# Kernel tuning notes

Hardware: AMD Instinct MI355X
Metric: run time of the kernel (lower is better)

Reference implementation:

```python
import jax, jax.numpy as jnp
import numpy as np

ALPHA = 10.0
DELTA = 0.0005
N = 16777216  # array_length


def setup_inputs() -> dict:
    key = jax.random.key(0)
    k1, k2 = jax.random.split(key)
    # learned parameter: in the original module this is initialized to linspace(0,1,N);
    # we use uniform [0,1] so the piecewise-linear search path is non-degenerate.
    indices = jax.random.uniform(k1, (N,), dtype=jnp.float32)
    array = jax.random.normal(k2, (N,), dtype=jnp.float32)
    return {"indices": indices, "array": array}


def reference(indices, array):
    # clamp learned knot positions to [0, 1]
    clamped = jnp.clip(indices, 0.0, 1.0)
    # piecewise-linear function f with x-knots = clamped, y-values = array.
    # jnp.interp requires ascending knots, so sort (x, y) pairs by x.
    order = jnp.argsort(clamped)
    xs = clamped[order]
    ys = array[order]
    # vectorized version of the per-index loop:
    #   left_item = f(clamped[i-1] + delta), this_item = f(clamped[i] - delta)
    q_left = clamped[:-1] + DELTA   # [N-1]
    q_this = clamped[1:] - DELTA    # [N-1]
    f_left = jnp.interp(q_left, xs, ys)
    f_this = jnp.interp(q_this, xs, ys)
    gap = jnp.maximum(f_left - f_this, 0.0)
    return ALPHA * jnp.sum(gap)
```

## Files before the change

kernel.cpp:

```cpp
#include <hip/hip_runtime.h>
#include <stdint.h>

#define ALPHA_C 10.0f
#define DELTA_C 0.0005f

typedef unsigned long long u64;
typedef unsigned u32;
typedef unsigned short u16;

#define KB2   (1u << 22)
#define NREG  8192
#define FPR   512
#define NBK   4096
#define RPB   2
#define FPB   1024
#define CAPB  4800
#define ACHUNK 32768
#define Q38MAX ((1ULL << 38) - 1)

#define OLDKB (1u << 22)
#define SCAN_BLOCKS 1024
#define SCAN_TPB 256
#define SCAN_PER_THREAD 16

__device__ __forceinline__ float clamp01(float x) {
    return fminf(fmaxf(x, 0.0f), 1.0f);
}
__device__ __forceinline__ u64 q38_of(float x) {
    double d = (double)clamp01(x) * 274877906944.0;
    u64 q = (u64)d;
    return q > Q38MAX ? Q38MAX : q;
}
__device__ __forceinline__ u16 f2bf(float f) {
    u32 b = __float_as_uint(f);
    return (u16)((b + 0x8000u) >> 16);
}
__device__ __forceinline__ float bf2f(u32 h) {
    return __uint_as_float(h << 16);
}


__global__ void __launch_bounds__(256) k_hist(const float* __restrict__ ind,
                                              u32* __restrict__ cnt8k, int n) {
    __shared__ u32 lh[NREG];
    for (int k = threadIdx.x; k < (int)NREG; k += 256) lh[k] = 0;
    __syncthreads();
    int stride = gridDim.x * blockDim.x;
    for (int i = blockIdx.x * blockDim.x + threadIdx.x; i < n; i += stride)
        atomicAdd(&lh[(u32)(q38_of(ind[i]) >> 25)], 1u);
    __syncthreads();
    for (int k = threadIdx.x; k < (int)NREG; k += 256) {
        u32 v = lh[k];
        if (v) atomicAdd(&cnt8k[k], v);
    }
}

__global__ void __launch_bounds__(1024) k_scan8k(u32* __restrict__ cnt8k) {
    __shared__ u32 lds[1024];
    int tid = threadIdx.x;
    int base = tid * 8;
    u32 v[8]; u32 tot = 0;
#pragma unroll
    for (int k = 0; k < 8; ++k) { v[k] = cnt8k[base + k]; tot += v[k]; }
    lds[tid] = tot;
    __syncthreads();
    u32 x = tot;
    for (int s = 1; s < 1024; s <<= 1) {
        u32 y = (tid >= s) ? lds[tid - s] : 0u;
        __syncthreads();
        x += y; lds[tid] = x;
        __syncthreads();
    }
    u32 run = x - tot;
#pragma unroll
    for (int k = 0; k < 8; ++k) { u32 c = v[k]; cnt8k[base + k] = run; run += c; }
}

__global__ void k_prep(const u32* __restrict__ cnt8k, u32* __restrict__ bcur) {
    int b = blockIdx.x * 256 + threadIdx.x;
    if (b < (int)NBK) bcur[b] = cnt8k[b * RPB];
}

__global__ void __launch_bounds__(256) k_bucket(const float* __restrict__ ind,
                                                u32* __restrict__ bcur,
                                                u64* __restrict__ rec, int n) {
    __shared__ u32 hist[NBK];
    __shared__ u32 base[NBK];
    int cbase = blockIdx.x * ACHUNK;
    for (u32 k = threadIdx.x; k < (u32)NBK; k += 256) hist[k] = 0;
    __syncthreads();
    for (int k = threadIdx.x; k < ACHUNK; k += 256) {
        int i = cbase + k;
        if (i >= n) break;
        u32 bk = (u32)(q38_of(ind[i]) >> 26);
        atomicAdd(&hist[bk], 1u);
    }
    __syncthreads();
    for (u32 k = threadIdx.x; k < (u32)NBK; k += 256) {
        u32 h = hist[k];
        base[k] = h ? atomicAdd(&bcur[k], h) : 0u;
    }
    __syncthreads();
    for (int k = threadIdx.x; k < ACHUNK; k += 256) {
        int i = cbase + k;
        if (i >= n) break;
        u64 q = q38_of(ind[i]);
        u32 bk = (u32)(q >> 26);
        u32 d = atomicAdd(&base[bk], 1u);
        rec[d] = (q << 24) | (u64)(u32)i;
    }
}

__global__ void __launch_bounds__(256) k_group_fine(const u32* __restrict__ cnt8k,
                                                    const float* __restrict__ arr,
                                                    u16* __restrict__ foff16,
                                                    u64* __restrict__ rec, int n) {
    __shared__ u64 srec[CAPB];
    __shared__ u32 sc[FPB];
    __shared__ u32 lad[256];
    int b = blockIdx.x;
    u32 S = cnt8k[b * RPB];
    u32 E = (b * RPB + RPB < (int)NREG) ? cnt8k[b * RPB + RPB] : (u32)n;
    u32 cnt = E - S; if (cnt > CAPB) cnt = CAPB;
    for (u32 j = threadIdx.x; j < cnt; j += 256) srec[j] = rec[S + j];
    for (u32 f = threadIdx.x; f < (u32)FPB; f += 256) sc[f] = 0;
    __syncthreads();
    for (u32 j = threadIdx.x; j < cnt; j += 256) {
        u32 fb = (u32)(srec[j] >> 40) & (FPB - 1);
        atomicAdd(&sc[fb], 1u);
    }
    __syncthreads();
    u32 c0 = sc[threadIdx.x * 4 + 0], c1 = sc[threadIdx.x * 4 + 1];
    u32 c2 = sc[threadIdx.x * 4 + 2], c3 = sc[threadIdx.x * 4 + 3];
    u32 tsum = c0 + c1 + c2 + c3;
    lad[threadIdx.x] = tsum;
    __syncthreads();
    u32 x = tsum;
    for (int st = 1; st < 256; st <<= 1) {
        u32 y = (threadIdx.x >= (u32)st) ? lad[threadIdx.x - st] : 0u;
        __syncthreads();
        x += y; lad[threadIdx.x] = x;
        __syncthreads();
    }
    u32 ex = x - tsum;
    u32 e0 = ex, e1 = ex + c0, e2 = ex + c0 + c1, e3 = ex + c0 + c1 + c2;
    sc[threadIdx.x * 4 + 0] = e0; sc[threadIdx.x * 4 + 1] = e1;
    sc[threadIdx.x * 4 + 2] = e2; sc[threadIdx.x * 4 + 3] = e3;
    __syncthreads();
    {
        u32 fb0 = threadIdx.x * 4;
        u32 rs0 = sc[fb0 & ~511u];
        u32 gb  = (u32)b * FPB + fb0;
        foff16[gb + 0] = (u16)(e0 + c0 - rs0);
        foff16[gb + 1] = (u16)(e1 + c1 - rs0);
        foff16[gb + 2] = (u16)(e2 + c2 - rs0);
        foff16[gb + 3] = (u16)(e3 + c3 - rs0);
    }
    __syncthreads();
    for (u32 j = threadIdx.x; j < cnt; j += 256) {
        u64 v = srec[j];
        u32 fb  = (u32)(v >> 40) & (FPB - 1);
        u32 i   = (u32)(v & 0xFFFFFFu);
        u32 xlo = (u32)(v >> 24) & 0xFFFFu;
        u32 ybf = f2bf(arr[i]);
        u32 pos = atomicAdd(&sc[fb], 1u);
        rec[S + pos] = ((u64)xlo << 40) | ((u64)ybf << 24) | (u64)i;
    }
}

__device__ __forceinline__ void bucket_range(u32 b, const u32* __restrict__ cnt8k,
                                             const u16* __restrict__ foff16,
                                             u32* s, u32* e) {
    u32 r = b >> 9;
    u32 rbase = cnt8k[r];
    u32 lb = b & (FPR - 1);
    *s = rbase + (lb ? (u32)foff16[b - 1] : 0u);
    *e = rbase + (u32)foff16[b];
}

__device__ float feval_q(u64 qq, const u32* __restrict__ cnt8k,
                         const u16* __restrict__ foff16, const u64* __restrict__ fdata) {
    u32 qb = (u32)(qq >> 16);
    u32 ql = (u32)(qq & 0xFFFFu);
    u32 s, e;
    bucket_range(qb, cnt8k, foff16, &s, &e);
    long long loK = -1;
    u64 hiK = ~0ULL;
    float loY = 0.0f, hiY = 0.0f;
    for (u32 p = s; p < e; ++p) {
        u64 d = fdata[p];
        u32 xlo = (u32)(d >> 40);
        u64 key = ((((u64)qb << 16) | xlo) << 24) | (d & 0xFFFFFFULL);
        float y = bf2f((u32)(d >> 24) & 0xFFFFu);
        if (xlo <= ql) { if ((long long)key >= loK) { loK = (long long)key; loY = y; } }
        else           { if (key < hiK)             { hiK = key;            hiY = y; } }
    }
    if (loK < 0) {
        u32 bl = qb;
        while (bl > 0) {
            --bl;
            u32 s2, e2;
            bucket_range(bl, cnt8k, foff16, &s2, &e2);
            if (e2 > s2) {
                for (u32 p = s2; p < e2; ++p) {
                    u64 d = fdata[p];
                    u64 key = ((((u64)bl << 16) | (d >> 40)) << 24) | (d & 0xFFFFFFULL);
                    if ((long long)key >= loK) { loK = (long long)key; loY = bf2f((u32)(d >> 24) & 0xFFFFu); }
                }
                break;
            }
        }
    }
    if (hiK == ~0ULL) {
        u32 br = qb;
        while (br < KB2 - 1) {
            ++br;
            u32 s2, e2;
            bucket_range(br, cnt8k, foff16, &s2, &e2);
            if (e2 > s2) {
                for (u32 p = s2; p < e2; ++p) {
                    u64 d = fdata[p];
                    u64 key = ((((u64)br << 16) | (d >> 40)) << 24) | (d & 0xFFFFFFULL);
                    if (key < hiK) { hiK = key; hiY = bf2f((u32)(d >> 24) & 0xFFFFu); }
                }
                break;
            }
        }
    }
    if (loK < 0) return hiY;
    if (hiK == ~0ULL) return loY;
    u64 loQ = (u64)loK >> 24;
    u64 hiQ = hiK >> 24;
    if (hiQ == loQ) return loY;
    float dq = (float)(qq - loQ);
    float dd = (float)(hiQ - loQ);
    return loY + (dq / dd) * (hiY - loY);
}

__global__ void __launch_bounds__(512) k_eval(const u32* __restrict__ cnt8k,
        const u16* __restrict__ foff16, const u64* __restrict__ fdata,
        u32* __restrict__ oval, int n) {
    __shared__ u32 fend[FPR];
    int r = blockIdx.x;
    u32 s = cnt8k[r];
    u32 e = (r + 1 < (int)NREG) ? cnt8k[r + 1] : (u32)n;
    fend[threadIdx.x] = s + (u32)foff16[r * FPR + threadIdx.x];
    __syncthreads();
    for (u32 t = s + threadIdx.x; t < e; t += 512) {
        u64 d = fdata[t];
        u32 lo = 0;
#pragma unroll
        for (u32 st = 256; st; st >>= 1) if (t >= fend[lo + st - 1]) lo += st;
        u64 xq = (((u64)((u32)r * FPR + lo)) << 16) | (d >> 40);
        u32 i = (u32)(d & 0xFFFFFFu);
        float x = (float)((double)xq * 3.63797880709171295e-12);
        float qpf = x + DELTA_C;
        float qmf = x - DELTA_C;
        u64 qp = q38_of(qpf);
        u64 qm = q38_of(qmf);
        float fp = feval_q(qp, cnt8k, foff16, fdata);
        float fm = feval_q(qm, cnt8k, foff16, fdata);
        oval[i] = ((u32)f2bf(fp) << 16) | (u32)f2bf(fm);
    }
}

__global__ void __launch_bounds__(256) k_pair2(const u32* __restrict__ oval,
                                               float* __restrict__ out, int n) {
    int stride = gridDim.x * blockDim.x;
    float sum = 0.0f;
    for (int j = blockIdx.x * blockDim.x + threadIdx.x; j < n - 1; j += stride) {
        u32 a = oval[j], b = oval[j + 1];
        sum += fmaxf(bf2f(a >> 16) - bf2f(b & 0xFFFFu), 0.0f);
    }
    float w = sum;
    for (int s = 32; s > 0; s >>= 1) w += __shfl_down(w, s, 64);
    __shared__ float wsum[4];
    if ((threadIdx.x & 63) == 0) wsum[threadIdx.x >> 6] = w;
    __syncthreads();
    if (threadIdx.x == 0)
        atomicAdd(out, ALPHA_C * (wsum[0] + wsum[1] + wsum[2] + wsum[3]));
}


__device__ __forceinline__ int bucket_of(float x) {
    int b = (int)(x * (float)OLDKB);
    b = b < 0 ? 0 : b;
    b = b > (int)OLDKB - 1 ? (int)OLDKB - 1 : b;
    return b;
}

__global__ void scan1(u32* __restrict__ off, u32* __restrict__ bsums) {
    __shared__ u32 lds[SCAN_TPB];
    int base = blockIdx.x * (SCAN_TPB * SCAN_PER_THREAD) + threadIdx.x * SCAN_PER_THREAD;
    u32 v[SCAN_PER_THREAD];
    u32 tot = 0;
#pragma unroll
    for (int k = 0; k < SCAN_PER_THREAD; ++k) { v[k] = off[base + k]; tot += v[k]; }
    lds[threadIdx.x] = tot;
    __syncthreads();
    u32 x = tot;
    for (int s = 1; s < SCAN_TPB; s <<= 1) {
        u32 y = (threadIdx.x >= (u32)s) ? lds[threadIdx.x - s] : 0u;
        __syncthreads();
        x += y; lds[threadIdx.x] = x;
        __syncthreads();
    }
    if (threadIdx.x == SCAN_TPB - 1) bsums[blockIdx.x] = x;
    u32 run = x - tot;
#pragma unroll
    for (int k = 0; k < SCAN_PER_THREAD; ++k) { u32 c = v[k]; off[base + k] = run; run += c; }
}

__global__ void scan2(u32* __restrict__ bsums) {
    __shared__ u32 lds[SCAN_BLOCKS];
    int tid = threadIdx.x;
    u32 v = bsums[tid];
    lds[tid] = v;
    __syncthreads();
    u32 x = v;
    for (int s = 1; s < SCAN_BLOCKS; s <<= 1) {
        u32 y = (tid >= s) ? lds[tid - s] : 0u;
        __syncthreads();
        x += y; lds[tid] = x;
        __syncthreads();
    }
    bsums[tid] = x - v;
}

__global__ void scan3(u32* __restrict__ off, const u32* __restrict__ bsums) {
    int base = blockIdx.x * (SCAN_TPB * SCAN_PER_THREAD);
    u32 add = bsums[blockIdx.x];
#pragma unroll
    for (int k = 0; k < SCAN_PER_THREAD; ++k)
        off[base + k * SCAN_TPB + threadIdx.x] += add;
}

__global__ void hist_kernel(const float* __restrict__ ind, u32* __restrict__ off, int n) {
    int i = blockIdx.x * blockDim.x + threadIdx.x;
    if (i < n) atomicAdd(&off[bucket_of(clamp01(ind[i]))], 1u);
}

__global__ void scatter_kernel(const float* __restrict__ ind, const float* __restrict__ arr,
                               u32* __restrict__ off, float2* __restrict__ buck, int n) {
    int i = blockIdx.x * blockDim.x + threadIdx.x;
    if (i < n) {
        float x = clamp01(ind[i]);
        u32 p = atomicAdd(&off[bucket_of(x)], 1u);
        buck[p] = make_float2(x, arr[i]);
    }
}

__device__ float feval(float q, const u32* __restrict__ off, const float2* __restrict__ buck) {
    int b = bucket_of(q);
    u32 s = (b == 0) ? 0u : off[b - 1];
    u32 e = off[b];
    float loX = -1e30f, loY = 0.0f, hiX = 1e30f, hiY = 0.0f;
    for (u32 u = s; u < e; ++u) {
        float2 p = buck[u];
        if (p.x <= q) { if (p.x >= loX) { loX = p.x; loY = p.y; } }
        else          { if (p.x <  hiX) { hiX = p.x; hiY = p.y; } }
    }
    if (loX == -1e30f) {
        int bl = b;
        while (bl > 0) {
            --bl;
            u32 s2 = (bl == 0) ? 0u : off[bl - 1];
            u32 e2 = off[bl];
            if (e2 > s2) {
                for (u32 u = s2; u < e2; ++u) {
                    float2 p = buck[u];
                    if (p.x >= loX) { loX = p.x; loY = p.y; }
                }
                break;
            }
        }
    }
    if (hiX == 1e30f) {
        int br = b;
        while (br < (int)OLDKB - 1) {
            ++br;
            u32 s2 = off[br - 1];
            u32 e2 = off[br];
            if (e2 > s2) {
                for (u32 u = s2; u < e2; ++u) {
                    float2 p = buck[u];
                    if (p.x < hiX) { hiX = p.x; hiY = p.y; }
                }
                break;
            }
        }
    }
    if (loX == -1e30f) return hiY;
    if (hiX ==  1e30f) return loY;
    return loY + (q - loX) * (hiY - loY) / (hiX - loX);
}

__global__ void query_kernel(const float* __restrict__ ind, const u32* __restrict__ off,
                             const float2* __restrict__ buck, float* __restrict__ out, int nterm) {
    int j = blockIdx.x * blockDim.x + threadIdx.x;
    float term = 0.0f;
    if (j < nterm) {
        float c0 = clamp01(ind[j]);
        float c1 = clamp01(ind[j + 1]);
        float fa = feval(c0 + DELTA_C, off, buck);
        float fb = feval(c1 - DELTA_C, off, buck);
        term = fmaxf(fa - fb, 0.0f);
    }
    float w = term;
    for (int s = 32; s > 0; s >>= 1) w += __shfl_down(w, s, 64);
    __shared__ float wsum[4];
    if ((threadIdx.x & 63) == 0) wsum[threadIdx.x >> 6] = w;
    __syncthreads();
    if (threadIdx.x == 0) atomicAdd(out, ALPHA_C * (wsum[0] + wsum[1] + wsum[2] + wsum[3]));
}


extern "C" void kernel_launch(void* const* d_in, const int* in_sizes, int n_in,
                              void* d_out, int out_size, void* d_ws, size_t ws_size,
                              hipStream_t stream) {
    const float* ind = (const float*)d_in[0];
    const float* arr = (const float*)d_in[1];
    float* out = (float*)d_out;
    int n = in_sizes[0];

    const int tpb = 256;
    int nblk = (n + tpb - 1) / tpb;
    uint8_t* w = (uint8_t*)d_ws;

    const size_t FOFF_SZ = (size_t)KB2 * 2;
    const size_t AUX = (size_t)1 << 20;
    size_t SZ8 = (size_t)n * 8, SZ4 = (size_t)n * 4;
    size_t base = FOFF_SZ + AUX;
    size_t need = base + SZ8 + SZ4;

    if (n <= (1 << 24) && ws_size >= need) {
        u16* foff16 = (u16*)w;
        u32* cnt8k  = (u32*)(w + FOFF_SZ);
        u32* bcur   = (u32*)(w + FOFF_SZ + 32768);
        u64* rec    = (u64*)(w + base);
        u32* oval   = (u32*)(w + base + SZ8);

        hipMemsetAsync(cnt8k, 0, NREG * 4, stream);
        hipMemsetAsync(out, 0, sizeof(float) * (size_t)out_size, stream);

        int abks = (n + ACHUNK - 1) / ACHUNK;
        k_hist<<<512, 256, 0, stream>>>(ind, cnt8k, n);
        k_scan8k<<<1, 1024, 0, stream>>>(cnt8k);
        k_prep<<<(NBK + 255) / 256, 256, 0, stream>>>(cnt8k, bcur);
        k_bucket<<<abks, 256, 0, stream>>>(ind, bcur, rec, n);
        k_group_fine<<<NBK, 256, 0, stream>>>(cnt8k, arr, foff16, rec, n);
        k_eval<<<NREG, 512, 0, stream>>>(cnt8k, foff16, rec, oval, n);
        k_pair2<<<2048, 256, 0, stream>>>(oval, out, n);
    } else {
        const size_t FO = (size_t)OLDKB * 4;
        u32* off = (u32*)w;
        u32* bsums = (u32*)(w + FO);
        float2* buck = (float2*)(w + FO + 4096);

        hipMemsetAsync(off, 0, FO, stream);
        hipMemsetAsync(out, 0, sizeof(float) * (size_t)out_size, stream);

        hist_kernel<<<nblk, tpb, 0, stream>>>(ind, off, n);
        scan1<<<SCAN_BLOCKS, SCAN_TPB, 0, stream>>>(off, bsums);
        scan2<<<1, SCAN_BLOCKS, 0, stream>>>(bsums);
        scan3<<<SCAN_BLOCKS, SCAN_TPB, 0, stream>>>(off, bsums);
        scatter_kernel<<<nblk, tpb, 0, stream>>>(ind, arr, off, buck, n);
        int nterm = n - 1;
        query_kernel<<<(nterm + tpb - 1) / tpb, tpb, 0, stream>>>(ind, off, buck, out, nterm);
    }
}
```

Measured before the change: 1.774 ms.

## Fully sort fine buckets and evaluate interp by rank with windowed offsets

Each fine bucket is now fully sorted in shared memory with an insertion sort, so lookups can find the rank of a query by counting keys at or below it in its bucket. The neighbouring knots are then the adjacent entries in the sorted array, which removes the min/max scans and the outward searches across empty buckets. k_eval loads bucket offsets for a window of nearby regions into shared memory. The y value is now gathered during bucketing rather than in the grouping pass. This relies on queries staying within the loaded window and on buckets being small enough for insertion sort to be cheap. It also reuses the oval buffer's memory for recy.

Result: slower. 1.869 ms (+5.4%).

```diff
diff --git a/kernel.cpp b/kernel.cpp
--- a/kernel.cpp
+++ b/kernel.cpp
@@ -16,6 +16,8 @@
 #define FPB   1024
 #define CAPB  4800
 #define ACHUNK 32768
+#define WR    5
+#define WMAXB ((2 * WR + 1) * FPR)
 #define Q38MAX ((1ULL << 38) - 1)
 
 #define OLDKB (1u << 22)
@@ -82,8 +84,10 @@
 }
 
 __global__ void __launch_bounds__(256) k_bucket(const float* __restrict__ ind,
+                                                const float* __restrict__ arr,
                                                 u32* __restrict__ bcur,
-                                                u64* __restrict__ rec, int n) {
+                                                u64* __restrict__ rec,
+                                                u16* __restrict__ recy, int n) {
     __shared__ u32 hist[NBK];
     __shared__ u32 base[NBK];
     int cbase = blockIdx.x * ACHUNK;
@@ -108,25 +112,26 @@
         u32 bk = (u32)(q >> 26);
         u32 d = atomicAdd(&base[bk], 1u);
         rec[d] = (q << 24) | (u64)(u32)i;
+        recy[d] = f2bf(arr[i]);
     }
 }
 
 __global__ void __launch_bounds__(256) k_group_fine(const u32* __restrict__ cnt8k,
-                                                    const float* __restrict__ arr,
+                                                    const u16* __restrict__ recy,
                                                     u16* __restrict__ foff16,
                                                     u64* __restrict__ rec, int n) {
-    __shared__ u64 srec[CAPB];
+    __shared__ u64 s2[CAPB];
+    __shared__ u16 sy[CAPB];
     __shared__ u32 sc[FPB];
     __shared__ u32 lad[256];
     int b = blockIdx.x;
     u32 S = cnt8k[b * RPB];
     u32 E = (b * RPB + RPB < (int)NREG) ? cnt8k[b * RPB + RPB] : (u32)n;
     u32 cnt = E - S; if (cnt > CAPB) cnt = CAPB;
-    for (u32 j = threadIdx.x; j < cnt; j += 256) srec[j] = rec[S + j];
     for (u32 f = threadIdx.x; f < (u32)FPB; f += 256) sc[f] = 0;
     __syncthreads();
     for (u32 j = threadIdx.x; j < cnt; j += 256) {
-        u32 fb = (u32)(srec[j] >> 40) & (FPB - 1);
+        u32 fb = (u32)(rec[S + j] >> 40) & (FPB - 1);
         atomicAdd(&sc[fb], 1u);
     }
     __syncthreads();
@@ -158,79 +163,52 @@
     }
     __syncthreads();
     for (u32 j = threadIdx.x; j < cnt; j += 256) {
-        u64 v = srec[j];
-        u32 fb  = (u32)(v >> 40) & (FPB - 1);
+        u64 v = rec[S + j];
+        u32 fb = (u32)(v >> 40) & (FPB - 1);
+        u32 p = atomicAdd(&sc[fb], 1u);
+        s2[p] = v;
+        sy[p] = recy[S + j];
+    }
+    __syncthreads();
+    for (u32 f = threadIdx.x; f < (u32)FPB; f += 256) {
+        u32 st = f ? sc[f - 1] : 0u;
+        u32 en = sc[f];
+        for (u32 a = st + 1; a < en; ++a) {
+            u64 key = s2[a]; u16 ky = sy[a]; u32 m = a;
+            while (m > st && s2[m - 1] > key) { s2[m] = s2[m - 1]; sy[m] = sy[m - 1]; --m; }
+            s2[m] = key; sy[m] = ky;
+        }
+    }
+    __syncthreads();
+    for (u32 j = threadIdx.x; j < cnt; j += 256) {
+        u64 v = s2[j];
         u32 i   = (u32)(v & 0xFFFFFFu);
         u32 xlo = (u32)(v >> 24) & 0xFFFFu;
-        u32 ybf = f2bf(arr[i]);
-        u32 pos = atomicAdd(&sc[fb], 1u);
-        rec[S + pos] = ((u64)xlo << 40) | ((u64)ybf << 24) | (u64)i;
-    }
-}
-
-__device__ __forceinline__ void bucket_range(u32 b, const u32* __restrict__ cnt8k,
-                                             const u16* __restrict__ foff16,
-                                             u32* s, u32* e) {
-    u32 r = b >> 9;
-    u32 rbase = cnt8k[r];
-    u32 lb = b & (FPR - 1);
-    *s = rbase + (lb ? (u32)foff16[b - 1] : 0u);
-    *e = rbase + (u32)foff16[b];
-}
-
-__device__ float feval_q(u64 qq, const u32* __restrict__ cnt8k,
-                         const u16* __restrict__ foff16, const u64* __restrict__ fdata) {
-    u32 qb = (u32)(qq >> 16);
+        u32 ybf = (u32)sy[j];
+        rec[S + j] = ((u64)xlo << 40) | ((u64)ybf << 24) | (u64)i;
+    }
+}
+
+__device__ __forceinline__ float feval2(u64 qq, u32 baseB, u32 nw,
+                                        const u32* pos,
+                                        const u64* __restrict__ fdata, u32 n) {
+    u32 wb = (u32)(qq >> 16) - baseB;
     u32 ql = (u32)(qq & 0xFFFFu);
-    u32 s, e;
-    bucket_range(qb, cnt8k, foff16, &s, &e);
-    long long loK = -1;
-    u64 hiK = ~0ULL;
-    float loY = 0.0f, hiY = 0.0f;
-    for (u32 p = s; p < e; ++p) {
-        u64 d = fdata[p];
-        u32 xlo = (u32)(d >> 40);
-        u64 key = ((((u64)qb << 16) | xlo) << 24) | (d & 0xFFFFFFULL);
-        float y = bf2f((u32)(d >> 24) & 0xFFFFu);
-        if (xlo <= ql) { if ((long long)key >= loK) { loK = (long long)key; loY = y; } }
-        else           { if (key < hiK)             { hiK = key;            hiY = y; } }
-    }
-    if (loK < 0) {
-        u32 bl = qb;
-        while (bl > 0) {
-            --bl;
-            u32 s2, e2;
-            bucket_range(bl, cnt8k, foff16, &s2, &e2);
-            if (e2 > s2) {
-                for (u32 p = s2; p < e2; ++p) {
-                    u64 d = fdata[p];
-                    u64 key = ((((u64)bl << 16) | (d >> 40)) << 24) | (d & 0xFFFFFFULL);
-                    if ((long long)key >= loK) { loK = (long long)key; loY = bf2f((u32)(d >> 24) & 0xFFFFu); }
-                }
-                break;
-            }
-        }
-    }
-    if (hiK == ~0ULL) {
-        u32 br = qb;
-        while (br < KB2 - 1) {
-            ++br;
-            u32 s2, e2;
-            bucket_range(br, cnt8k, foff16, &s2, &e2);
-            if (e2 > s2) {
-                for (u32 p = s2; p < e2; ++p) {
-                    u64 d = fdata[p];
-                    u64 key = ((((u64)br << 16) | (d >> 40)) << 24) | (d & 0xFFFFFFULL);
-                    if (key < hiK) { hiK = key; hiY = bf2f((u32)(d >> 24) & 0xFFFFu); }
-                }
-                break;
-            }
-        }
-    }
-    if (loK < 0) return hiY;
-    if (hiK == ~0ULL) return loY;
-    u64 loQ = (u64)loK >> 24;
-    u64 hiQ = hiK >> 24;
+    u32 bs = pos[wb], be = pos[wb + 1];
+    u32 c = 0;
+    for (u32 p = bs; p < be; ++p)
+        c += ((u32)(fdata[p] >> 40) <= ql) ? 1u : 0u;
+    u32 P = bs + c;
+    if (P == 0)  return bf2f((u32)(fdata[0] >> 24) & 0xFFFFu);
+    if (P >= n)  return bf2f((u32)(fdata[n - 1] >> 24) & 0xFFFFu);
+    u64 dlo = fdata[P - 1];
+    u64 dhi = fdata[P];
+    u32 wl = wb; while (wl > 0 && pos[wl] > P - 1) --wl;
+    u32 wh = wb; while (wh + 1 < nw && pos[wh + 1] <= P) ++wh;
+    u64 loQ = (((u64)(baseB + wl)) << 16) | (dlo >> 40);
+    u64 hiQ = (((u64)(baseB + wh)) << 16) | (dhi >> 40);
+    float loY = bf2f((u32)(dlo >> 24) & 0xFFFFu);
+    float hiY = bf2f((u32)(dhi >> 24) & 0xFFFFu);
     if (hiQ == loQ) return loY;
     float dq = (float)(qq - loQ);
     float dd = (float)(hiQ - loQ);
@@ -240,17 +218,27 @@
 __global__ void __launch_bounds__(512) k_eval(const u32* __restrict__ cnt8k,
         const u16* __restrict__ foff16, const u64* __restrict__ fdata,
         u32* __restrict__ oval, int n) {
-    __shared__ u32 fend[FPR];
+    __shared__ u32 pos[WMAXB + 1];
     int r = blockIdx.x;
+    int r0 = r - WR; if (r0 < 0) r0 = 0;
+    int r1 = r + WR; if (r1 > (int)NREG - 1) r1 = (int)NREG - 1;
+    u32 nw = (u32)(r1 - r0 + 1) << 9;
+    u32 baseB = (u32)r0 << 9;
+    for (u32 k = threadIdx.x; k < nw; k += 512) {
+        u32 reg = (u32)r0 + (k >> 9);
+        pos[1 + k] = cnt8k[reg] + (u32)foff16[(reg << 9) + (k & 511u)];
+    }
+    if (threadIdx.x == 0) pos[0] = cnt8k[r0];
+    __syncthreads();
     u32 s = cnt8k[r];
     u32 e = (r + 1 < (int)NREG) ? cnt8k[r + 1] : (u32)n;
-    fend[threadIdx.x] = s + (u32)foff16[r * FPR + threadIdx.x];
-    __syncthreads();
+    u32 selfoff = ((u32)(r - r0)) << 9;
     for (u32 t = s + threadIdx.x; t < e; t += 512) {
         u64 d = fdata[t];
         u32 lo = 0;
 #pragma unroll
-        for (u32 st = 256; st; st >>= 1) if (t >= fend[lo + st - 1]) lo += st;
+        for (u32 st = 256; st; st >>= 1)
+            if (t >= pos[selfoff + lo + st]) lo += st;
         u64 xq = (((u64)((u32)r * FPR + lo)) << 16) | (d >> 40);
         u32 i = (u32)(d & 0xFFFFFFu);
         float x = (float)((double)xq * 3.63797880709171295e-12);
@@ -258,9 +246,10 @@
         float qmf = x - DELTA_C;
         u64 qp = q38_of(qpf);
         u64 qm = q38_of(qmf);
-        float fp = feval_q(qp, cnt8k, foff16, fdata);
-        float fm = feval_q(qm, cnt8k, foff16, fdata);
-        oval[i] = ((u32)f2bf(fp) << 16) | (u32)f2bf(fm);
+        float fp = feval2(qp, baseB, nw, pos, fdata, (u32)n);
+        float fm = feval2(qm, baseB, nw, pos, fdata, (u32)n);
+        u32 o = ((u32)f2bf(fp) << 16) | (u32)f2bf(fm);
+        __builtin_nontemporal_store(o, &oval[i]);
     }
 }
 
@@ -438,6 +427,7 @@
         u32* cnt8k  = (u32*)(w + FOFF_SZ);
         u32* bcur   = (u32*)(w + FOFF_SZ + 32768);
         u64* rec    = (u64*)(w + base);
+        u16* recy   = (u16*)(w + base + SZ8);
         u32* oval   = (u32*)(w + base + SZ8);
 
         hipMemsetAsync(cnt8k, 0, NREG * 4, stream);
@@ -447,8 +437,8 @@
         k_hist<<<512, 256, 0, stream>>>(ind, cnt8k, n);
         k_scan8k<<<1, 1024, 0, stream>>>(cnt8k);
         k_prep<<<(NBK + 255) / 256, 256, 0, stream>>>(cnt8k, bcur);
-        k_bucket<<<abks, 256, 0, stream>>>(ind, bcur, rec, n);
-        k_group_fine<<<NBK, 256, 0, stream>>>(cnt8k, arr, foff16, rec, n);
+        k_bucket<<<abks, 256, 0, stream>>>(ind, arr, bcur, rec, recy, n);
+        k_group_fine<<<NBK, 256, 0, stream>>>(cnt8k, recy, foff16, rec, n);
         k_eval<<<NREG, 512, 0, stream>>>(cnt8k, foff16, rec, oval, n);
         k_pair2<<<2048, 256, 0, stream>>>(oval, out, n);
     } else {
```

## Fuse fine grouping and evaluation into one LDS-resident per-bucket kernel

Applied to the files above, without the earlier changes.

Replaces the separate fine-grouping and evaluation kernels with a single kernel. Each block loads its coarse bucket's records into shared memory, counting-sorts them by fine bucket, and answers every query whose shifted position lands in that bucket. Queries are found by scanning the records of neighbouring buckets, so lookups hit LDS instead of global memory. This removes the global rewrite of records and the foff16 table, and splits the output into two u16 arrays. The cost is rescanning neighbour-bucket records, global fallback searches when a bucket edge is empty, and a cap (CAPE) on records that fit in shared memory.

New measurement: 5.776 ms. 226% more time.

```diff
diff --git a/kernel.cpp b/kernel.cpp
--- a/kernel.cpp
+++ b/kernel.cpp
@@ -8,13 +8,11 @@
 typedef unsigned u32;
 typedef unsigned short u16;
 
-#define KB2   (1u << 22)
 #define NREG  8192
-#define FPR   512
+#define NB    4096
 #define NBK   4096
-#define RPB   2
-#define FPB   1024
-#define CAPB  4800
+#define FPB2  1024
+#define CAPE  4680
 #define ACHUNK 32768
 #define Q38MAX ((1ULL << 38) - 1)
 
@@ -78,7 +76,7 @@
 
 __global__ void k_prep(const u32* __restrict__ cnt8k, u32* __restrict__ bcur) {
     int b = blockIdx.x * 256 + threadIdx.x;
-    if (b < (int)NBK) bcur[b] = cnt8k[b * RPB];
+    if (b < (int)NBK) bcur[b] = cnt8k[b * 2];
 }
 
 __global__ void __launch_bounds__(256) k_bucket(const float* __restrict__ ind,
@@ -111,167 +109,168 @@
     }
 }
 
-__global__ void __launch_bounds__(256) k_group_fine(const u32* __restrict__ cnt8k,
-                                                    const float* __restrict__ arr,
-                                                    u16* __restrict__ foff16,
-                                                    u64* __restrict__ rec, int n) {
-    __shared__ u64 srec[CAPB];
-    __shared__ u32 sc[FPB];
-    __shared__ u32 lad[256];
-    int b = blockIdx.x;
-    u32 S = cnt8k[b * RPB];
-    u32 E = (b * RPB + RPB < (int)NREG) ? cnt8k[b * RPB + RPB] : (u32)n;
-    u32 cnt = E - S; if (cnt > CAPB) cnt = CAPB;
-    for (u32 j = threadIdx.x; j < cnt; j += 256) srec[j] = rec[S + j];
-    for (u32 f = threadIdx.x; f < (u32)FPB; f += 256) sc[f] = 0;
-    __syncthreads();
-    for (u32 j = threadIdx.x; j < cnt; j += 256) {
-        u32 fb = (u32)(srec[j] >> 40) & (FPB - 1);
-        atomicAdd(&sc[fb], 1u);
-    }
-    __syncthreads();
-    u32 c0 = sc[threadIdx.x * 4 + 0], c1 = sc[threadIdx.x * 4 + 1];
-    u32 c2 = sc[threadIdx.x * 4 + 2], c3 = sc[threadIdx.x * 4 + 3];
-    u32 tsum = c0 + c1 + c2 + c3;
-    lad[threadIdx.x] = tsum;
-    __syncthreads();
-    u32 x = tsum;
-    for (int st = 1; st < 256; st <<= 1) {
-        u32 y = (threadIdx.x >= (u32)st) ? lad[threadIdx.x - st] : 0u;
-        __syncthreads();
-        x += y; lad[threadIdx.x] = x;
-        __syncthreads();
-    }
-    u32 ex = x - tsum;
-    u32 e0 = ex, e1 = ex + c0, e2 = ex + c0 + c1, e3 = ex + c0 + c1 + c2;
-    sc[threadIdx.x * 4 + 0] = e0; sc[threadIdx.x * 4 + 1] = e1;
-    sc[threadIdx.x * 4 + 2] = e2; sc[threadIdx.x * 4 + 3] = e3;
-    __syncthreads();
+__global__ void __launch_bounds__(512) k_eval_f(const u32* __restrict__ cnt8k,
+        const float* __restrict__ arr, const u64* __restrict__ rec,
+        u16* __restrict__ ovalp, u16* __restrict__ ovalm, int n) {
+    __shared__ u64 srec[CAPE];
+    __shared__ u16 sy[CAPE];
+    __shared__ u32 sc[FPB2];
+    __shared__ u32 lad[512];
+    int bid = blockIdx.x;
+    int b = (bid & 7) * (NB / 8) + (bid >> 3);
+    u32 S = cnt8k[b * 2];
+    u32 E = (b * 2 + 2 < (int)NREG) ? cnt8k[b * 2 + 2] : (u32)n;
+    u32 cnt = E - S; if (cnt > (u32)CAPE) cnt = CAPE;
+    for (u32 f = threadIdx.x; f < (u32)FPB2; f += 512) sc[f] = 0;
+    __syncthreads();
+    for (u32 j = threadIdx.x; j < cnt; j += 512)
+        atomicAdd(&sc[(u32)(rec[S + j] >> 40) & (FPB2 - 1)], 1u);
+    __syncthreads();
+    u32 c0 = sc[threadIdx.x * 2], c1 = sc[threadIdx.x * 2 + 1];
+    u32 ts = c0 + c1;
+    lad[threadIdx.x] = ts;
+    __syncthreads();
+    u32 xx = ts;
+    for (int st = 1; st < 512; st <<= 1) {
+        u32 yv = (threadIdx.x >= (u32)st) ? lad[threadIdx.x - st] : 0u;
+        __syncthreads();
+        xx += yv; lad[threadIdx.x] = xx;
+        __syncthreads();
+    }
+    u32 ex = xx - ts;
+    sc[threadIdx.x * 2] = ex;
+    sc[threadIdx.x * 2 + 1] = ex + c0;
+    __syncthreads();
+    for (u32 j = threadIdx.x; j < cnt; j += 512) {
+        u64 v = rec[S + j];
+        u32 fb = (u32)(v >> 40) & (FPB2 - 1);
+        u32 p = atomicAdd(&sc[fb], 1u);
+        if (p < (u32)CAPE) { srec[p] = v; sy[p] = f2bf(arr[(u32)(v & 0xFFFFFFu)]); }
+    }
+    __syncthreads();
+
+    auto evalq = [&](u64 q) -> float {
+        u64 qk = (q << 24) | 0xFFFFFFull;
+        u32 fb = (u32)(q >> 16) & (FPB2 - 1);
+        u32 bs = fb ? sc[fb - 1] : 0u;
+        u32 be = sc[fb];
+        u64 loK = 0, hiK = ~0ULL;
+        int loI = -1, hiI = -1;
+        for (u32 p = bs; p < be; ++p) {
+            u64 k = srec[p];
+            if (k <= qk) { if (loI < 0 || k >= loK) { loK = k; loI = (int)p; } }
+            else         { if (k <  hiK)            { hiK = k; hiI = (int)p; } }
+        }
+        if (loI < 0) {
+            int f = (int)fb;
+            while (f > 0) {
+                --f;
+                u32 s2 = f ? sc[f - 1] : 0u, e2 = sc[f];
+                if (e2 > s2) {
+                    for (u32 p = s2; p < e2; ++p) { u64 k = srec[p]; if (loI < 0 || k >= loK) { loK = k; loI = (int)p; } }
+                    break;
+                }
+            }
+        }
+        if (hiI < 0) {
+            int f = (int)fb;
+            while (f + 1 < (int)FPB2) {
+                ++f;
+                u32 s2 = sc[f - 1], e2 = sc[f];
+                if (e2 > s2) {
+                    for (u32 p = s2; p < e2; ++p) { u64 k = srec[p]; if (hiI < 0 || k < hiK) { hiK = k; hiI = (int)p; } }
+                    break;
+                }
+            }
+        }
+        float loY = 0.0f, hiY = 0.0f;
+        bool haveLo = (loI >= 0), haveHi = (hiI >= 0);
+        if (haveLo) loY = bf2f((u32)sy[loI]);
+        if (haveHi) hiY = bf2f((u32)sy[hiI]);
+        if (!haveLo) {
+            int nb = b; u32 ee = S; u32 gi = 0; bool g = false;
+            while (nb > 0 && !g) {
+                --nb;
+                u32 ss = cnt8k[nb * 2];
+                for (u32 p = ss; p < ee; ++p) {
+                    u64 k = rec[p];
+                    if (!g || k >= loK) { loK = k; gi = (u32)(k & 0xFFFFFFu); g = true; }
+                }
+                ee = ss;
+            }
+            if (g) { loY = bf2f((u32)f2bf(arr[gi])); haveLo = true; }
+        }
+        if (!haveHi) {
+            int nb = b; u32 ss = E; u32 gi = 0; bool g = false;
+            while (nb < (int)NB - 1 && !g) {
+                ++nb;
+                u32 ee2 = (nb * 2 + 2 < (int)NREG) ? cnt8k[nb * 2 + 2] : (u32)n;
+                for (u32 p = ss; p < ee2; ++p) {
+                    u64 k = rec[p];
+                    if (!g || k < hiK) { hiK = k; gi = (u32)(k & 0xFFFFFFu); g = true; }
+                }
+                ss = ee2;
+            }
+            if (g) { hiY = bf2f((u32)f2bf(arr[gi])); haveHi = true; }
+        }
+        if (!haveLo) return haveHi ? hiY : 0.0f;
+        if (!haveHi) return loY;
+        u64 loQ = loK >> 24, hiQ = hiK >> 24;
+        if (hiQ == loQ) return loY;
+        float dq = (float)(q - loQ);
+        float dd = (float)(hiQ - loQ);
+        return loY + (dq / dd) * (hiY - loY);
+    };
+
     {
-        u32 fb0 = threadIdx.x * 4;
-        u32 rs0 = sc[fb0 & ~511u];
-        u32 gb  = (u32)b * FPB + fb0;
-        foff16[gb + 0] = (u16)(e0 + c0 - rs0);
-        foff16[gb + 1] = (u16)(e1 + c1 - rs0);
-        foff16[gb + 2] = (u16)(e2 + c2 - rs0);
-        foff16[gb + 3] = (u16)(e3 + c3 - rs0);
-    }
-    __syncthreads();
-    for (u32 j = threadIdx.x; j < cnt; j += 256) {
-        u64 v = srec[j];
-        u32 fb  = (u32)(v >> 40) & (FPB - 1);
-        u32 i   = (u32)(v & 0xFFFFFFu);
-        u32 xlo = (u32)(v >> 24) & 0xFFFFu;
-        u32 ybf = f2bf(arr[i]);
-        u32 pos = atomicAdd(&sc[fb], 1u);
-        rec[S + pos] = ((u64)xlo << 40) | ((u64)ybf << 24) | (u64)i;
-    }
-}
-
-__device__ __forceinline__ void bucket_range(u32 b, const u32* __restrict__ cnt8k,
-                                             const u16* __restrict__ foff16,
-                                             u32* s, u32* e) {
-    u32 r = b >> 9;
-    u32 rbase = cnt8k[r];
-    u32 lb = b & (FPR - 1);
-    *s = rbase + (lb ? (u32)foff16[b - 1] : 0u);
-    *e = rbase + (u32)foff16[b];
-}
-
-__device__ float feval_q(u64 qq, const u32* __restrict__ cnt8k,
-                         const u16* __restrict__ foff16, const u64* __restrict__ fdata) {
-    u32 qb = (u32)(qq >> 16);
-    u32 ql = (u32)(qq & 0xFFFFu);
-    u32 s, e;
-    bucket_range(qb, cnt8k, foff16, &s, &e);
-    long long loK = -1;
-    u64 hiK = ~0ULL;
-    float loY = 0.0f, hiY = 0.0f;
-    for (u32 p = s; p < e; ++p) {
-        u64 d = fdata[p];
-        u32 xlo = (u32)(d >> 40);
-        u64 key = ((((u64)qb << 16) | xlo) << 24) | (d & 0xFFFFFFULL);
-        float y = bf2f((u32)(d >> 24) & 0xFFFFu);
-        if (xlo <= ql) { if ((long long)key >= loK) { loK = (long long)key; loY = y; } }
-        else           { if (key < hiK)             { hiK = key;            hiY = y; } }
-    }
-    if (loK < 0) {
-        u32 bl = qb;
-        while (bl > 0) {
-            --bl;
-            u32 s2, e2;
-            bucket_range(bl, cnt8k, foff16, &s2, &e2);
-            if (e2 > s2) {
-                for (u32 p = s2; p < e2; ++p) {
-                    u64 d = fdata[p];
-                    u64 key = ((((u64)bl << 16) | (d >> 40)) << 24) | (d & 0xFFFFFFULL);
-                    if ((long long)key >= loK) { loK = (long long)key; loY = bf2f((u32)(d >> 24) & 0xFFFFu); }
-                }
-                break;
-            }
-        }
-    }
-    if (hiK == ~0ULL) {
-        u32 br = qb;
-        while (br < KB2 - 1) {
-            ++br;
-            u32 s2, e2;
-            bucket_range(br, cnt8k, foff16, &s2, &e2);
-            if (e2 > s2) {
-                for (u32 p = s2; p < e2; ++p) {
-                    u64 d = fdata[p];
-                    u64 key = ((((u64)br << 16) | (d >> 40)) << 24) | (d & 0xFFFFFFULL);
-                    if (key < hiK) { hiK = key; hiY = bf2f((u32)(d >> 24) & 0xFFFFu); }
-                }
-                break;
-            }
-        }
-    }
-    if (loK < 0) return hiY;
-    if (hiK == ~0ULL) return loY;
-    u64 loQ = (u64)loK >> 24;
-    u64 hiQ = hiK >> 24;
-    if (hiQ == loQ) return loY;
-    float dq = (float)(qq - loQ);
-    float dd = (float)(hiQ - loQ);
-    return loY + (dq / dd) * (hiY - loY);
-}
-
-__global__ void __launch_bounds__(512) k_eval(const u32* __restrict__ cnt8k,
-        const u16* __restrict__ foff16, const u64* __restrict__ fdata,
-        u32* __restrict__ oval, int n) {
-    __shared__ u32 fend[FPR];
-    int r = blockIdx.x;
-    u32 s = cnt8k[r];
-    u32 e = (r + 1 < (int)NREG) ? cnt8k[r + 1] : (u32)n;
-    fend[threadIdx.x] = s + (u32)foff16[r * FPR + threadIdx.x];
-    __syncthreads();
-    for (u32 t = s + threadIdx.x; t < e; t += 512) {
-        u64 d = fdata[t];
-        u32 lo = 0;
-#pragma unroll
-        for (u32 st = 256; st; st >>= 1) if (t >= fend[lo + st - 1]) lo += st;
-        u64 xq = (((u64)((u32)r * FPR + lo)) << 16) | (d >> 40);
-        u32 i = (u32)(d & 0xFFFFFFu);
-        float x = (float)((double)xq * 3.63797880709171295e-12);
-        float qpf = x + DELTA_C;
-        float qmf = x - DELTA_C;
-        u64 qp = q38_of(qpf);
-        u64 qm = q38_of(qmf);
-        float fp = feval_q(qp, cnt8k, foff16, fdata);
-        float fm = feval_q(qm, cnt8k, foff16, fdata);
-        oval[i] = ((u32)f2bf(fp) << 16) | (u32)f2bf(fm);
-    }
-}
-
-__global__ void __launch_bounds__(256) k_pair2(const u32* __restrict__ oval,
+        int s0, s1;
+        if (b == (int)NB - 1)      { s0 = NB - 4; s1 = NB - 1; }
+        else if (b >= 2)           { s0 = b - 3; if (s0 < 0) s0 = 0; s1 = b - 2; }
+        else                       { s0 = 1; s1 = 0; }
+        if (s0 <= s1) {
+            u32 a0 = cnt8k[s0 * 2];
+            u32 a1 = (s1 * 2 + 2 < (int)NREG) ? cnt8k[s1 * 2 + 2] : (u32)n;
+            for (u32 j = a0 + threadIdx.x; j < a1; j += 512) {
+                u64 v = rec[j];
+                u64 qs = v >> 24;
+                float xv = (float)((double)qs * 3.63797880709171295e-12);
+                u64 qp = q38_of(xv + DELTA_C);
+                if ((u32)(qp >> 26) == (u32)b) {
+                    float fp = evalq(qp);
+                    ovalp[(u32)(v & 0xFFFFFFu)] = f2bf(fp);
+                }
+            }
+        }
+    }
+    {
+        int s0, s1;
+        if (b == 0)                 { s0 = 0; s1 = 3; }
+        else if (b <= (int)NB - 3)  { s0 = b + 2; s1 = b + 3; if (s1 > (int)NB - 1) s1 = NB - 1; }
+        else                        { s0 = 1; s1 = 0; }
+        if (s0 <= s1) {
+            u32 a0 = cnt8k[s0 * 2];
+            u32 a1 = (s1 * 2 + 2 < (int)NREG) ? cnt8k[s1 * 2 + 2] : (u32)n;
+            for (u32 j = a0 + threadIdx.x; j < a1; j += 512) {
+                u64 v = rec[j];
+                u64 qs = v >> 24;
+                float xv = (float)((double)qs * 3.63797880709171295e-12);
+                u64 qm = q38_of(xv - DELTA_C);
+                if ((u32)(qm >> 26) == (u32)b) {
+                    float fm = evalq(qm);
+                    ovalm[(u32)(v & 0xFFFFFFu)] = f2bf(fm);
+                }
+            }
+        }
+    }
+}
+
+__global__ void __launch_bounds__(256) k_pair2(const u16* __restrict__ ovalp,
+                                               const u16* __restrict__ ovalm,
                                                float* __restrict__ out, int n) {
     int stride = gridDim.x * blockDim.x;
     float sum = 0.0f;
-    for (int j = blockIdx.x * blockDim.x + threadIdx.x; j < n - 1; j += stride) {
-        u32 a = oval[j], b = oval[j + 1];
-        sum += fmaxf(bf2f(a >> 16) - bf2f(b & 0xFFFFu), 0.0f);
-    }
+    for (int j = blockIdx.x * blockDim.x + threadIdx.x; j < n - 1; j += stride)
+        sum += fmaxf(bf2f((u32)ovalp[j]) - bf2f((u32)ovalm[j + 1]), 0.0f);
     float w = sum;
     for (int s = 32; s > 0; s >>= 1) w += __shfl_down(w, s, 64);
     __shared__ float wsum[4];
@@ -427,18 +426,16 @@
     int nblk = (n + tpb - 1) / tpb;
     uint8_t* w = (uint8_t*)d_ws;
 
-    const size_t FOFF_SZ = (size_t)KB2 * 2;
-    const size_t AUX = (size_t)1 << 20;
-    size_t SZ8 = (size_t)n * 8, SZ4 = (size_t)n * 4;
-    size_t base = FOFF_SZ + AUX;
-    size_t need = base + SZ8 + SZ4;
+    const size_t AUXSZ = (size_t)1 << 20;
+    size_t SZ8 = (size_t)n * 8, SZ2 = (size_t)n * 2;
+    size_t need = AUXSZ + SZ8 + 2 * SZ2;
 
     if (n <= (1 << 24) && ws_size >= need) {
-        u16* foff16 = (u16*)w;
-        u32* cnt8k  = (u32*)(w + FOFF_SZ);
-        u32* bcur   = (u32*)(w + FOFF_SZ + 32768);
-        u64* rec    = (u64*)(w + base);
-        u32* oval   = (u32*)(w + base + SZ8);
+        u32* cnt8k  = (u32*)w;
+        u32* bcur   = (u32*)(w + 32768);
+        u64* rec    = (u64*)(w + AUXSZ);
+        u16* ovalp  = (u16*)(w + AUXSZ + SZ8);
+        u16* ovalm  = (u16*)(w + AUXSZ + SZ8 + SZ2);
 
         hipMemsetAsync(cnt8k, 0, NREG * 4, stream);
         hipMemsetAsync(out, 0, sizeof(float) * (size_t)out_size, stream);
@@ -448,9 +445,8 @@
         k_scan8k<<<1, 1024, 0, stream>>>(cnt8k);
         k_prep<<<(NBK + 255) / 256, 256, 0, stream>>>(cnt8k, bcur);
         k_bucket<<<abks, 256, 0, stream>>>(ind, bcur, rec, n);
-        k_group_fine<<<NBK, 256, 0, stream>>>(cnt8k, arr, foff16, rec, n);
-        k_eval<<<NREG, 512, 0, stream>>>(cnt8k, foff16, rec, oval, n);
-        k_pair2<<<2048, 256, 0, stream>>>(oval, out, n);
+        k_eval_f<<<NB, 512, 0, stream>>>(cnt8k, arr, rec, ovalp, ovalm, n);
+        k_pair2<<<2048, 256, 0, stream>>>(ovalp, ovalm, out, n);
     } else {
         const size_t FO = (size_t)OLDKB * 4;
         u32* off = (u32*)w;
```
